# Kernel optimization log

Hardware: AMD Instinct MI355X
Metric: run time of the kernel (lower is better)

The kernel has to match this reference:

```python
import jax, jax.numpy as jnp
import numpy as np

D_MODEL = 1024
NUM_HEADS = 16
HEAD_DIM = D_MODEL // NUM_HEADS
SCALE = 1.0 / (HEAD_DIM ** 0.5)


def setup_inputs() -> dict:
    key = jax.random.key(0)
    ks = jax.random.split(key, 5)
    std = 1.0 / np.sqrt(D_MODEL)
    x = jax.random.normal(ks[0], (2, 2048, D_MODEL), dtype=jnp.float32)
    Wq = jax.random.normal(ks[1], (D_MODEL, D_MODEL), dtype=jnp.float32) * std
    Wk = jax.random.normal(ks[2], (D_MODEL, D_MODEL), dtype=jnp.float32) * std
    Wv = jax.random.normal(ks[3], (D_MODEL, D_MODEL), dtype=jnp.float32) * std
    Wo = jax.random.normal(ks[4], (D_MODEL, D_MODEL), dtype=jnp.float32) * std
    zeros = jnp.zeros((D_MODEL,), dtype=jnp.float32)
    return {"x": x, "Wq": Wq, "bq": zeros, "Wk": Wk, "bk": zeros,
            "Wv": Wv, "bv": zeros, "Wo": Wo, "bo": zeros}


def reference(x, Wq, bq, Wk, bk, Wv, bv, Wo, bo):
    B, S, D = x.shape
    H, hd = NUM_HEADS, HEAD_DIM
    # Linear projections (torch Linear: y = x @ W.T + b)
    q = (x @ Wq.T + bq).reshape(B, S, H, hd).transpose(0, 2, 1, 3)  # [B,H,S,hd]
    k = (x @ Wk.T + bk).reshape(B, S, H, hd).transpose(0, 2, 1, 3)
    v = (x @ Wv.T + bv).reshape(B, S, H, hd).transpose(0, 2, 1, 3)
    scores = jnp.einsum('bhqd,bhkd->bhqk', q, k) * SCALE  # [B,H,S,S]
    causal = jnp.tril(jnp.ones((S, S), dtype=bool))
    scores = jnp.where(causal, scores, -jnp.inf)
    attn = jax.nn.softmax(scores, axis=-1)
    out = jnp.einsum('bhqk,bhkd->bhqd', attn, v)  # [B,H,S,hd]
    out = out.transpose(0, 2, 1, 3).reshape(B, S, D)
    return out @ Wo.T + bo
```

## Files before the change

kernel.cpp:

```cpp
#include <hip/hip_runtime.h>
#include <hip/hip_bf16.h>


typedef __attribute__((ext_vector_type(8))) short short8;
typedef __attribute__((ext_vector_type(4))) float f32x4;
typedef __attribute__((ext_vector_type(8))) unsigned short u16x8;
typedef __attribute__((ext_vector_type(4))) unsigned short u16x4;

#define QSCALE 0.1803368801111244f
#define MFMA16(a, b, c) __builtin_amdgcn_mfma_f32_16x16x32_bf16(a, b, c, 0, 0, 0)

__device__ __forceinline__ unsigned short f2bf(float f) {
  unsigned int u = __float_as_uint(f);
  u += 0x7fffu + ((u >> 16) & 1u);
  return (unsigned short)(u >> 16);
}

__device__ __forceinline__ void gload_lds16(const void* g, void* l) {
  __builtin_amdgcn_global_load_lds(
      (const __attribute__((address_space(1))) unsigned int*)g,
      (__attribute__((address_space(3))) unsigned int*)l, 16, 0, 0);
}

__global__ __launch_bounds__(256) void convert_all_kernel(
    const float* __restrict__ x, const float* __restrict__ wq,
    const float* __restrict__ wk, const float* __restrict__ wv,
    const float* __restrict__ wo, unsigned short* __restrict__ xb,
    unsigned short* __restrict__ wqkv, unsigned short* __restrict__ wob) {
  const int b = blockIdx.x, tid = threadIdx.x;
  const float* src;
  unsigned short* dst;
  int i;
  if (b < 4096) { src = x; dst = xb; i = b * 256 + tid; }
  else {
    const int r = b - 4096, seg = r >> 10;
    i = (r & 1023) * 256 + tid;
    src = seg == 0 ? wq : (seg == 1 ? wk : (seg == 2 ? wv : wo));
    dst = seg == 3 ? wob : wqkv + (size_t)seg * 1048576;
  }
  float4 v = ((const float4*)src)[i];
  u16x4 o = {f2bf(v.x), f2bf(v.y), f2bf(v.z), f2bf(v.w)};
  *(u16x4*)(dst + (size_t)i * 4) = o;
}

__device__ __forceinline__ void gemm128_mainloop(
    const unsigned short* __restrict__ A, const unsigned short* __restrict__ B,
    int tm, int tn, unsigned short* As, unsigned short* Bs, f32x4 acc[4][4]) {
  const int tid = threadIdx.x;
  const int w = tid >> 6, l = tid & 63;
  const int wr = (w >> 1) * 64, wc = (w & 1) * 64;
  const int srow = l >> 2;
  const int schunk = (l & 3) * 8;
  const int rl = l & 15, kl = (l >> 4) * 8;
  const int K = 1024;
  for (int k0 = 0; k0 < K; k0 += 32) {
#pragma unroll
    for (int c = 0; c < 2; ++c) {
      const int rowb = w * 32 + c * 16;
      gload_lds16(A + (size_t)(tm + rowb + srow) * K + k0 + schunk, As + rowb * 32);
      gload_lds16(B + (size_t)(tn + rowb + srow) * K + k0 + schunk, Bs + rowb * 32);
    }
    __syncthreads();
    short8 af[4], bf[4];
#pragma unroll
    for (int m = 0; m < 4; ++m) af[m] = *(const short8*)&As[(wr + m * 16 + rl) * 32 + kl];
#pragma unroll
    for (int n = 0; n < 4; ++n) bf[n] = *(const short8*)&Bs[(wc + n * 16 + rl) * 32 + kl];
#pragma unroll
    for (int m = 0; m < 4; ++m)
#pragma unroll
      for (int n = 0; n < 4; ++n)
        acc[m][n] = MFMA16(af[m], bf[n], acc[m][n]);
    __syncthreads();
  }
}

__global__ __launch_bounds__(256) void gemm_qkv_kernel(
    const unsigned short* __restrict__ xb, const unsigned short* __restrict__ wqkv,
    const float* __restrict__ bq, const float* __restrict__ bk, const float* __restrict__ bv,
    unsigned short* __restrict__ Qb, unsigned short* __restrict__ Kb,
    unsigned short* __restrict__ VTb) {
  __shared__ unsigned short As[128 * 32], Bs[128 * 32];
  f32x4 acc[4][4] = {};
  const int flat = blockIdx.x;
  const int xcd = flat & 7, loc = flat >> 3;
  const int bn = xcd * 3 + loc % 3, bm = loc / 3;
  const int tm = bm * 128, tn = bn * 128;
  gemm128_mainloop(xb, wqkv, tm, tn, As, Bs, acc);

  const int tid = threadIdx.x, w = tid >> 6, l = tid & 63;
  const int wr = (w >> 1) * 64, wc = (w & 1) * 64;
  const int rl = l & 15, hi = l >> 4;
  const int proj = tn >> 10;
  const float* bias = proj == 0 ? bq : (proj == 1 ? bk : bv);
#pragma unroll
  for (int m = 0; m < 4; ++m) {
    const int row0 = tm + wr + m * 16 + hi * 4;
    const int b2 = row0 >> 11, s2 = row0 & 2047;
#pragma unroll
    for (int n = 0; n < 4; ++n) {
      const int col = (tn & 1023) + wc + n * 16 + rl;
      const int h = col >> 6, d = col & 63;
      const float bi = bias[col];
      if (proj == 2) {
        u16x4 pv = {f2bf(acc[m][n][0] + bi), f2bf(acc[m][n][1] + bi),
                    f2bf(acc[m][n][2] + bi), f2bf(acc[m][n][3] + bi)};
        *(u16x4*)&VTb[((size_t)((b2 * 16 + h) * 64 + d)) * 2048 + s2] = pv;
      } else {
        const float sc = (proj == 0) ? QSCALE : 1.0f;
        unsigned short* dst = (proj == 0) ? Qb : Kb;
#pragma unroll
        for (int i = 0; i < 4; ++i)
          dst[((size_t)(b2 * 16 + h) * 2048 + (s2 + i)) * 64 + d] =
              f2bf((acc[m][n][i] + bi) * sc);
      }
    }
  }
}

template<bool DIAG>
__device__ __forceinline__ void softmax_pack(
    const f32x4 s[4], float& l_i, char* ps,
    int rl, int hi, int swz, int qrow, int kv0) {
  float p[4][4];
  float rs = 0.f;
#pragma unroll
  for (int f = 0; f < 4; ++f)
#pragma unroll
    for (int i = 0; i < 4; ++i) {
      float sv = s[f][i];
      if (DIAG) sv = (kv0 + f * 16 + hi * 4 + i <= qrow) ? sv : -1e30f;
      const float e = __builtin_amdgcn_exp2f(sv);
      p[f][i] = e;
      rs += e;
    }
  rs += __shfl_xor(rs, 16, 64);
  rs += __shfl_xor(rs, 32, 64);
  l_i += rs;
#pragma unroll
  for (int f = 0; f < 4; ++f) {
    u16x4 pv = {f2bf(p[f][0]), f2bf(p[f][1]), f2bf(p[f][2]), f2bf(p[f][3])};
    *(u16x4*)(ps + rl * 128 + ((f * 32 + hi * 8) ^ swz)) = pv;
  }
}

template<bool L_ON, bool L_DIAG, bool H_DIAG>
__device__ __forceinline__ void attn_stage(
    const char* kb, const char* vb, char* psH, char* psL,
    const short8 qfH[2], const short8 qfL[2],
    f32x4 oH[4], f32x4 oL[4], float& lH, float& lL,
    int rl, int hi, int swz, int qrH, int qrL, int kv0, int w) {
  const int fvH = H_DIAG ? (w + 1) : 4;
  f32x4 sH[4] = {}, sL[4] = {};
#pragma unroll
  for (int f = 0; f < 4; ++f) {
    if (H_DIAG && f >= fvH) continue;
    const char* rowp = kb + (f * 16 + rl) * 128;
#pragma unroll
    for (int kc = 0; kc < 2; ++kc) {
      short8 kf = *(const short8*)(rowp + ((kc * 64 + hi * 16) ^ swz));
      sH[f] = MFMA16(kf, qfH[kc], sH[f]);
      if (L_ON && (!L_DIAG || f < w + 1)) sL[f] = MFMA16(kf, qfL[kc], sL[f]);
    }
  }
  softmax_pack<H_DIAG>(sH, lH, psH, rl, hi, swz, qrH, kv0);
  if (L_ON) softmax_pack<L_DIAG>(sL, lL, psL, rl, hi, swz, qrL, kv0);

  const int kcvH = H_DIAG ? ((w >= 2) ? 2 : 1) : 2;
  const int kcvL = (L_ON && L_DIAG) ? ((w >= 2) ? 2 : 1) : 2;
#pragma unroll
  for (int kc = 0; kc < 2; ++kc) {
    if (H_DIAG && kc >= kcvH) continue;
    short8 paH = *(const short8*)(psH + rl * 128 + ((kc * 64 + hi * 16) ^ swz));
    const bool lpv = L_ON && kc < kcvL;
    short8 paL = {};
    if (lpv) paL = *(const short8*)(psL + rl * 128 + ((kc * 64 + hi * 16) ^ swz));
#pragma unroll
    for (int fd = 0; fd < 4; ++fd) {
      short8 vf = *(const short8*)(vb + (fd * 16 + rl) * 128 + ((kc * 64 + hi * 16) ^ swz));
      oH[fd] = MFMA16(vf, paH, oH[fd]);
      if (lpv) oL[fd] = MFMA16(vf, paL, oL[fd]);
    }
  }
}

__global__ __launch_bounds__(256) void flash_kernel(
    const unsigned short* __restrict__ Q, const unsigned short* __restrict__ K,
    const unsigned short* __restrict__ VT, unsigned short* __restrict__ AO) {
  __shared__ unsigned short KbS[2][64 * 64];
  __shared__ unsigned short VbS[2][64 * 64];
  __shared__ unsigned short PsS[4][2][16 * 64];

  const int tid = threadIdx.x;
  const int w = tid >> 6, l = tid & 63;
  const int rl = l & 15, hi = l >> 4;
  const int swz = (rl & 7) << 4;
  const int bid = blockIdx.x;
  const int g = bid & 7, r = bid >> 3;
  const int bh = g * 4 + (r & 3);
  const int pr = r >> 2;
  const int qtH = 31 - pr, qtL = pr;
  const size_t head_off = (size_t)bh * 2048 * 64;

  const int qrH = qtH * 64 + w * 16 + rl;
  const int qrL = qtL * 64 + w * 16 + rl;

  short8 qfH[2], qfL[2];
  {
    const unsigned short* qp = Q + head_off + (size_t)qrH * 64 + hi * 8;
    qfH[0] = *(const short8*)qp;
    qfH[1] = *(const short8*)(qp + 32);
    qp = Q + head_off + (size_t)qrL * 64 + hi * 8;
    qfL[0] = *(const short8*)qp;
    qfL[1] = *(const short8*)(qp + 32);
  }

  f32x4 oH[4] = {}, oL[4] = {};
  float lH = 0.f, lL = 0.f;

  const int sr = tid >> 2;
  const int swzW = (sr & 7) << 4;
  const int cb0 = (tid & 3) * 32;
  const int kwoff0 = sr * 128 + (cb0 ^ swzW);
  const int kwoff1 = sr * 128 + ((cb0 + 16) ^ swzW);
  const unsigned short* kbase = K + head_off + (size_t)sr * 64 + (tid & 3) * 16;
  const unsigned short* vbase = VT + ((size_t)(bh * 64 + sr)) * 2048 + (tid & 3) * 16;

  u16x8 kra = *(const u16x8*)kbase;
  u16x8 krb = *(const u16x8*)(kbase + 8);
  u16x8 vra = *(const u16x8*)vbase;
  u16x8 vrb = *(const u16x8*)(vbase + 8);
  {
    char* kd = (char*)KbS;
    char* vd = (char*)VbS;
    *(u16x8*)(kd + kwoff0) = kra;
    *(u16x8*)(kd + kwoff1) = krb;
    *(u16x8*)(vd + kwoff0) = vra;
    *(u16x8*)(vd + kwoff1) = vrb;
  }
  kra = *(const u16x8*)(kbase + 4096);
  krb = *(const u16x8*)(kbase + 4096 + 8);
  vra = *(const u16x8*)(vbase + 64);
  vrb = *(const u16x8*)(vbase + 64 + 8);
  __syncthreads();

  char* psH = (char*)&PsS[w][0][0];
  char* psL = (char*)&PsS[w][1][0];

  for (int t = 0; t <= qtH; ++t) {
    const int cur = t & 1;
    const char* kb = (const char*)KbS + cur * 8192;
    const char* vb = (const char*)VbS + cur * 8192;
    const int kv0 = t * 64;

    if (t < qtL)
      attn_stage<true, false, false>(kb, vb, psH, psL, qfH, qfL, oH, oL, lH, lL,
                                     rl, hi, swz, qrH, qrL, kv0, w);
    else if (t == qtL)
      attn_stage<true, true, false>(kb, vb, psH, psL, qfH, qfL, oH, oL, lH, lL,
                                    rl, hi, swz, qrH, qrL, kv0, w);
    else if (t < qtH)
      attn_stage<false, false, false>(kb, vb, psH, psL, qfH, qfL, oH, oL, lH, lL,
                                      rl, hi, swz, qrH, qrL, kv0, w);
    else
      attn_stage<false, false, true>(kb, vb, psH, psL, qfH, qfL, oH, oL, lH, lL,
                                     rl, hi, swz, qrH, qrL, kv0, w);

    if (t < qtH) {
      char* kd = (char*)KbS + (cur ^ 1) * 8192;
      char* vd = (char*)VbS + (cur ^ 1) * 8192;
      *(u16x8*)(kd + kwoff0) = kra;
      *(u16x8*)(kd + kwoff1) = krb;
      *(u16x8*)(vd + kwoff0) = vra;
      *(u16x8*)(vd + kwoff1) = vrb;
      if (t + 2 <= qtH) {
        const size_t ko = (size_t)(t + 2) * 4096;
        kra = *(const u16x8*)(kbase + ko);
        krb = *(const u16x8*)(kbase + ko + 8);
        vra = *(const u16x8*)(vbase + (t + 2) * 64);
        vrb = *(const u16x8*)(vbase + (t + 2) * 64 + 8);
      }
    }
    __syncthreads();
  }

  const float invH = 1.f / lH, invL = 1.f / lL;
  const size_t orowH = (size_t)(bh >> 4) * 2048 + qrH;
  const size_t orowL = (size_t)(bh >> 4) * 2048 + qrL;
  const int hcol = (bh & 15) * 64;
#pragma unroll
  for (int fd = 0; fd < 4; ++fd) {
    u16x4 a = {f2bf(oH[fd][0] * invH), f2bf(oH[fd][1] * invH),
               f2bf(oH[fd][2] * invH), f2bf(oH[fd][3] * invH)};
    *(u16x4*)&AO[orowH * 1024 + hcol + fd * 16 + hi * 4] = a;
    u16x4 b = {f2bf(oL[fd][0] * invL), f2bf(oL[fd][1] * invL),
               f2bf(oL[fd][2] * invL), f2bf(oL[fd][3] * invL)};
    *(u16x4*)&AO[orowL * 1024 + hcol + fd * 16 + hi * 4] = b;
  }
}

__global__ __launch_bounds__(256) void gemm_out_kernel(
    const unsigned short* __restrict__ AOb, const unsigned short* __restrict__ wob,
    const float* __restrict__ bo, float* __restrict__ out) {
  __shared__ unsigned short As[128 * 32], Bs[128 * 32];
  f32x4 acc[4][4] = {};
  const int flat = blockIdx.x;
  const int bn = flat & 7, bm = flat >> 3;
  const int tm = bm * 128, tn = bn * 128;
  gemm128_mainloop(AOb, wob, tm, tn, As, Bs, acc);
  const int tid = threadIdx.x, w = tid >> 6, l = tid & 63;
  const int wr = (w >> 1) * 64, wc = (w & 1) * 64;
  const int rl = l & 15, hi = l >> 4;
#pragma unroll
  for (int m = 0; m < 4; ++m) {
    const int row0 = tm + wr + m * 16 + hi * 4;
#pragma unroll
    for (int n = 0; n < 4; ++n) {
      const int col = tn + wc + n * 16 + rl;
      const float bo_ = bo[col];
#pragma unroll
      for (int i = 0; i < 4; ++i)
        out[(size_t)(row0 + i) * 1024 + col] = acc[m][n][i] + bo_;
    }
  }
}

extern "C" void kernel_launch(void* const* d_in, const int* in_sizes, int n_in,
                              void* d_out, int out_size, void* d_ws, size_t ws_size,
                              hipStream_t stream) {
  const float* x  = (const float*)d_in[0];
  const float* Wq = (const float*)d_in[1];
  const float* bq = (const float*)d_in[2];
  const float* Wk = (const float*)d_in[3];
  const float* bk = (const float*)d_in[4];
  const float* Wv = (const float*)d_in[5];
  const float* bv = (const float*)d_in[6];
  const float* Wo = (const float*)d_in[7];
  const float* bo = (const float*)d_in[8];
  float* out = (float*)d_out;

  unsigned short* ws = (unsigned short*)d_ws;
  unsigned short* XB   = ws;
  unsigned short* WQKV = ws + 4194304;
  unsigned short* WOB  = ws + 7340032;
  unsigned short* QB   = ws + 8388608;
  unsigned short* KB   = ws + 12582912;
  unsigned short* VTB  = ws + 16777216;
  unsigned short* AOB  = XB;

  convert_all_kernel<<<8192, 256, 0, stream>>>(x, Wq, Wk, Wv, Wo, XB, WQKV, WOB);
  gemm_qkv_kernel<<<768, 256, 0, stream>>>(XB, WQKV, bq, bk, bv, QB, KB, VTB);
  flash_kernel<<<512, 256, 0, stream>>>(QB, KB, VTB, AOB);
  gemm_out_kernel<<<256, 256, 0, stream>>>(AOB, WOB, bo, out);
}
```

Before: 200.9 us.

## Double-buffer GEMM LDS tiles, halve out-proj tile width, add MFMA priority hints

Replaces the single-buffered GEMM mainloop with a double-buffered one that issues global-to-LDS loads for the next K slice before computing the current one, removing one barrier per iteration and overlapping load latency with MFMA. The output projection now uses 128x64 tiles with 512 blocks and an XCD-aware block mapping, which improves CU occupancy for a grid that previously covered only 256 blocks. The flash kernel raises wave priority around its MFMA sections with s_setprio. The costs are double the LDS footprint in the GEMMs, and less B-tile reuse in the output GEMM.

```diff
diff --git a/kernel.cpp b/kernel.cpp
--- a/kernel.cpp
+++ b/kernel.cpp
@@ -43,36 +43,61 @@
   *(u16x4*)(dst + (size_t)i * 4) = o;
 }
 
-__device__ __forceinline__ void gemm128_mainloop(
+template<int NF>
+__device__ __forceinline__ void gemm_db_mainloop(
     const unsigned short* __restrict__ A, const unsigned short* __restrict__ B,
-    int tm, int tn, unsigned short* As, unsigned short* Bs, f32x4 acc[4][4]) {
+    int tm, int tn, unsigned short* As0, unsigned short* Bs0,
+    f32x4 (&acc)[4][NF]) {
+  constexpr int BN = NF * 32;
   const int tid = threadIdx.x;
   const int w = tid >> 6, l = tid & 63;
-  const int wr = (w >> 1) * 64, wc = (w & 1) * 64;
+  const int wr = (w >> 1) * 64, wc = (w & 1) * (BN / 2);
   const int srow = l >> 2;
   const int schunk = (l & 3) * 8;
   const int rl = l & 15, kl = (l >> 4) * 8;
   const int K = 1024;
+  unsigned short* As1 = As0 + 128 * 32;
+  unsigned short* Bs1 = Bs0 + BN * 32;
+
+#define STAGE_TILE(AP, BP, KOFF)                                               \
+  {                                                                            \
+    _Pragma("unroll") for (int c = 0; c < 2; ++c) {                            \
+      const int rowb = w * 32 + c * 16;                                        \
+      gload_lds16(A + (size_t)(tm + rowb + srow) * K + (KOFF) + schunk,        \
+                  (AP) + rowb * 32);                                           \
+    }                                                                          \
+    _Pragma("unroll") for (int c = 0; c < BN / 64; ++c) {                      \
+      const int rowb = w * (BN / 4) + c * 16;                                  \
+      gload_lds16(B + (size_t)(tn + rowb + srow) * K + (KOFF) + schunk,        \
+                  (BP) + rowb * 32);                                           \
+    }                                                                          \
+  }
+
+  STAGE_TILE(As0, Bs0, 0)
+  __syncthreads();
+  int p = 0;
   for (int k0 = 0; k0 < K; k0 += 32) {
-#pragma unroll
-    for (int c = 0; c < 2; ++c) {
-      const int rowb = w * 32 + c * 16;
-      gload_lds16(A + (size_t)(tm + rowb + srow) * K + k0 + schunk, As + rowb * 32);
-      gload_lds16(B + (size_t)(tn + rowb + srow) * K + k0 + schunk, Bs + rowb * 32);
-    }
-    __syncthreads();
-    short8 af[4], bf[4];
-#pragma unroll
-    for (int m = 0; m < 4; ++m) af[m] = *(const short8*)&As[(wr + m * 16 + rl) * 32 + kl];
-#pragma unroll
-    for (int n = 0; n < 4; ++n) bf[n] = *(const short8*)&Bs[(wc + n * 16 + rl) * 32 + kl];
+    unsigned short* Ac = p ? As1 : As0;
+    unsigned short* Bc = p ? Bs1 : Bs0;
+    if (k0 + 32 < K) {
+      unsigned short* An = p ? As0 : As1;
+      unsigned short* Bn = p ? Bs0 : Bs1;
+      STAGE_TILE(An, Bn, k0 + 32)
+    }
+    short8 af[4], bf[NF];
+#pragma unroll
+    for (int m = 0; m < 4; ++m) af[m] = *(const short8*)&Ac[(wr + m * 16 + rl) * 32 + kl];
+#pragma unroll
+    for (int n = 0; n < NF; ++n) bf[n] = *(const short8*)&Bc[(wc + n * 16 + rl) * 32 + kl];
 #pragma unroll
     for (int m = 0; m < 4; ++m)
 #pragma unroll
-      for (int n = 0; n < 4; ++n)
+      for (int n = 0; n < NF; ++n)
         acc[m][n] = MFMA16(af[m], bf[n], acc[m][n]);
     __syncthreads();
-  }
+    p ^= 1;
+  }
+#undef STAGE_TILE
 }
 
 __global__ __launch_bounds__(256) void gemm_qkv_kernel(
@@ -80,13 +105,13 @@
     const float* __restrict__ bq, const float* __restrict__ bk, const float* __restrict__ bv,
     unsigned short* __restrict__ Qb, unsigned short* __restrict__ Kb,
     unsigned short* __restrict__ VTb) {
-  __shared__ unsigned short As[128 * 32], Bs[128 * 32];
+  __shared__ unsigned short As[2 * 128 * 32], Bs[2 * 128 * 32];
   f32x4 acc[4][4] = {};
   const int flat = blockIdx.x;
   const int xcd = flat & 7, loc = flat >> 3;
   const int bn = xcd * 3 + loc % 3, bm = loc / 3;
   const int tm = bm * 128, tn = bn * 128;
-  gemm128_mainloop(xb, wqkv, tm, tn, As, Bs, acc);
+  gemm_db_mainloop<4>(xb, wqkv, tm, tn, As, Bs, acc);
 
   const int tid = threadIdx.x, w = tid >> 6, l = tid & 63;
   const int wr = (w >> 1) * 64, wc = (w & 1) * 64;
@@ -152,6 +177,7 @@
     int rl, int hi, int swz, int qrH, int qrL, int kv0, int w) {
   const int fvH = H_DIAG ? (w + 1) : 4;
   f32x4 sH[4] = {}, sL[4] = {};
+  __builtin_amdgcn_s_setprio(1);
 #pragma unroll
   for (int f = 0; f < 4; ++f) {
     if (H_DIAG && f >= fvH) continue;
@@ -163,11 +189,13 @@
       if (L_ON && (!L_DIAG || f < w + 1)) sL[f] = MFMA16(kf, qfL[kc], sL[f]);
     }
   }
+  __builtin_amdgcn_s_setprio(0);
   softmax_pack<H_DIAG>(sH, lH, psH, rl, hi, swz, qrH, kv0);
   if (L_ON) softmax_pack<L_DIAG>(sL, lL, psL, rl, hi, swz, qrL, kv0);
 
   const int kcvH = H_DIAG ? ((w >= 2) ? 2 : 1) : 2;
   const int kcvL = (L_ON && L_DIAG) ? ((w >= 2) ? 2 : 1) : 2;
+  __builtin_amdgcn_s_setprio(1);
 #pragma unroll
   for (int kc = 0; kc < 2; ++kc) {
     if (H_DIAG && kc >= kcvH) continue;
@@ -182,6 +210,7 @@
       if (lpv) oL[fd] = MFMA16(vf, paL, oL[fd]);
     }
   }
+  __builtin_amdgcn_s_setprio(0);
 }
 
 __global__ __launch_bounds__(256) void flash_kernel(
@@ -302,20 +331,21 @@
 __global__ __launch_bounds__(256) void gemm_out_kernel(
     const unsigned short* __restrict__ AOb, const unsigned short* __restrict__ wob,
     const float* __restrict__ bo, float* __restrict__ out) {
-  __shared__ unsigned short As[128 * 32], Bs[128 * 32];
-  f32x4 acc[4][4] = {};
+  __shared__ unsigned short As[2 * 128 * 32], Bs[2 * 64 * 32];
+  f32x4 acc[4][2] = {};
   const int flat = blockIdx.x;
-  const int bn = flat & 7, bm = flat >> 3;
-  const int tm = bm * 128, tn = bn * 128;
-  gemm128_mainloop(AOb, wob, tm, tn, As, Bs, acc);
+  const int xcd = flat & 7, loc = flat >> 3;
+  const int bn = xcd * 2 + (loc & 1), bm = loc >> 1;
+  const int tm = bm * 128, tn = bn * 64;
+  gemm_db_mainloop<2>(AOb, wob, tm, tn, As, Bs, acc);
   const int tid = threadIdx.x, w = tid >> 6, l = tid & 63;
-  const int wr = (w >> 1) * 64, wc = (w & 1) * 64;
+  const int wr = (w >> 1) * 64, wc = (w & 1) * 32;
   const int rl = l & 15, hi = l >> 4;
 #pragma unroll
   for (int m = 0; m < 4; ++m) {
     const int row0 = tm + wr + m * 16 + hi * 4;
 #pragma unroll
-    for (int n = 0; n < 4; ++n) {
+    for (int n = 0; n < 2; ++n) {
       const int col = tn + wc + n * 16 + rl;
       const float bo_ = bo[col];
 #pragma unroll
@@ -351,5 +381,5 @@
   convert_all_kernel<<<8192, 256, 0, stream>>>(x, Wq, Wk, Wv, Wo, XB, WQKV, WOB);
   gemm_qkv_kernel<<<768, 256, 0, stream>>>(XB, WQKV, bq, bk, bv, QB, KB, VTB);
   flash_kernel<<<512, 256, 0, stream>>>(QB, KB, VTB, AOB);
-  gemm_out_kernel<<<256, 256, 0, stream>>>(AOB, WOB, bo, out);
-}
+  gemm_out_kernel<<<512, 256, 0, stream>>>(AOB, WOB, bo, out);
+}
```

New measurement: 197.8 us. About the same (-1.5%).
